# Kernel optimization log

Measured on AMD Instinct MI355X. Metric: run time of the kernel, lower is better.

The kernel has to match this reference:

```python
import jax, jax.numpy as jnp
import numpy as np

B, N, DIM = 2, 2048, 1024
H, DH = 16, 64
INNER = H * DH
LN_EPS = 1e-5
ATTN_EPS = 1e-8
SCALE = DH ** -0.5


def setup_inputs() -> dict:
    key = jax.random.key(0)
    k1, k2, k3 = jax.random.split(key, 3)
    x = jax.random.normal(k1, (B, N, DIM), dtype=jnp.float32)
    ln_gamma = jnp.ones((DIM,), dtype=jnp.float32)
    ln_beta = jnp.zeros((DIM,), dtype=jnp.float32)
    w_qkv = jax.random.normal(k2, (DIM, 3 * INNER), dtype=jnp.float32) * 0.02
    w_out = jax.random.normal(k3, (INNER, DIM), dtype=jnp.float32) * 0.02
    b_out = jnp.zeros((DIM,), dtype=jnp.float32)
    return {"x": x, "ln_gamma": ln_gamma, "ln_beta": ln_beta,
            "w_qkv": w_qkv, "w_out": w_out, "b_out": b_out}


def reference(x, ln_gamma, ln_beta, w_qkv, w_out, b_out):
    # LayerNorm over last dim (biased variance, eps=1e-5)
    mu = jnp.mean(x, axis=-1, keepdims=True)
    var = jnp.var(x, axis=-1, keepdims=True)
    xn = (x - mu) * jax.lax.rsqrt(var + LN_EPS) * ln_gamma + ln_beta
    # QKV projection (no bias), split heads: b n (h d) -> b h n d
    qkv = xn @ w_qkv                                    # [B, N, 3*INNER]
    q, k, v = jnp.split(qkv, 3, axis=-1)
    split_heads = lambda t: t.reshape(B, N, H, DH).transpose(0, 2, 1, 3)
    q, k, v = split_heads(q), split_heads(k), split_heads(v)
    # 'softmax' attn_type: exp(scale * q k^T), normalized by row-sum + eps
    scores = jnp.einsum('bhnd,bhmd->bhnm', q, k) * SCALE   # [B, H, N, N]
    numer = jnp.exp(scores)
    denom = jnp.sum(numer, axis=-1, keepdims=True) + ATTN_EPS
    attn = numer / denom
    out = jnp.einsum('bhnm,bhmd->bhnd', attn, v)           # [B, H, N, DH]
    out = out.transpose(0, 2, 1, 3).reshape(B, N, INNER)   # b h n d -> b n (h d)
    return out @ w_out + b_out
```

## Files before the change

### kernel.cpp

```cpp
#include <hip/hip_runtime.h>
#include <hip/hip_bf16.h>

#define NB    2
#define SEQ   2048
#define DIM_  1024
#define NH    16
#define DHD   64
#define INNER 1024
#define ROWS  4096

typedef _Float16 half_t;
typedef __attribute__((ext_vector_type(4))) _Float16 half4;
typedef __attribute__((ext_vector_type(8))) _Float16 half8;
typedef __attribute__((ext_vector_type(4))) float f32x4;
typedef __attribute__((ext_vector_type(16))) float f32x16;
typedef __attribute__((ext_vector_type(2))) int int2v;
typedef __attribute__((ext_vector_type(4))) int int4v;

__device__ __forceinline__ void async16(const void* g, void* l) {
    __builtin_amdgcn_global_load_lds(
        (const __attribute__((address_space(1))) unsigned int*)g,
        (__attribute__((address_space(3))) unsigned int*)l, 16, 0, 0);
}

__device__ __forceinline__ float ldf(const void* p, size_t i, int isb) {
    if (isb) {
        unsigned int v = ((unsigned int)((const unsigned short*)p)[i]) << 16;
        return __uint_as_float(v);
    }
    return ((const float*)p)[i];
}

__global__ void detect_dtype(const unsigned short* x, int* flag) {
    int tid = threadIdx.x;
    int cnt = 0;
    for (int i = tid; i < 2048; i += 64) {
        float f = __uint_as_float(((unsigned int)x[2 * i]) << 16);
        float a = fabsf(f);
        if (a >= 0.0009765625f && a <= 16.0f) cnt++;
    }
    for (int off = 32; off > 0; off >>= 1) cnt += __shfl_down(cnt, off);
    if (tid == 0) flag[0] = (cnt > 1024) ? 1 : 0;
}

__global__ __launch_bounds__(256) void ln_kernel(const void* __restrict__ x,
                                                 const void* __restrict__ gamma,
                                                 const void* __restrict__ beta,
                                                 half_t* __restrict__ xn,
                                                 const int* __restrict__ flag) {
    int row = blockIdx.x;
    int isb = flag[0];
    int tid = threadIdx.x;
    float vals[4];
    float s = 0.f, ss = 0.f;
    if (!isb) {
        float4 xv = *(const float4*)((const float*)x + (size_t)row * DIM_ + tid * 4);
        vals[0] = xv.x; vals[1] = xv.y; vals[2] = xv.z; vals[3] = xv.w;
    } else {
        #pragma unroll
        for (int j = 0; j < 4; j++) vals[j] = ldf(x, (size_t)row * DIM_ + tid * 4 + j, isb);
    }
    #pragma unroll
    for (int j = 0; j < 4; j++) { s += vals[j]; ss += vals[j] * vals[j]; }
    __shared__ float red[2][4];
    for (int off = 32; off > 0; off >>= 1) {
        s += __shfl_down(s, off);
        ss += __shfl_down(ss, off);
    }
    int wid = tid >> 6;
    if ((tid & 63) == 0) { red[0][wid] = s; red[1][wid] = ss; }
    __syncthreads();
    if (tid == 0) {
        float S = 0.f, SS = 0.f;
        for (int w = 0; w < 4; w++) { S += red[0][w]; SS += red[1][w]; }
        float mu = S / 1024.f;
        float var = SS / 1024.f - mu * mu;
        red[0][0] = mu;
        red[1][0] = rsqrtf(var + 1e-5f);
    }
    __syncthreads();
    float mu = red[0][0], r = red[1][0];
    half4 o;
    #pragma unroll
    for (int j = 0; j < 4; j++) {
        int c = tid * 4 + j;
        float g = ldf(gamma, c, isb);
        float b = ldf(beta, c, isb);
        o[j] = (half_t)((vals[j] - mu) * r * g + b);
    }
    *(half4*)(xn + (size_t)row * DIM_ + tid * 4) = o;
}

__global__ __launch_bounds__(256) void wtrans(const void* __restrict__ W,
                                              half_t* __restrict__ WT,
                                              int K_, int N_,
                                              const int* __restrict__ flag) {
    __shared__ half_t T[64][72];
    int isb = flag[0];
    int k0 = blockIdx.y * 64, n0 = blockIdx.x * 64;
    int t = threadIdx.x;
    if (!isb) {
        #pragma unroll
        for (int p = 0; p < 4; p++) {
            int idx = p * 256 + t;
            int r = idx >> 4, c4 = (idx & 15) * 4;
            float4 xv = *(const float4*)((const float*)W + (size_t)(k0 + r) * N_ + n0 + c4);
            T[r][c4] = (half_t)xv.x; T[r][c4 + 1] = (half_t)xv.y;
            T[r][c4 + 2] = (half_t)xv.z; T[r][c4 + 3] = (half_t)xv.w;
        }
    } else {
        int c = t & 63, rw = t >> 6;
        #pragma unroll
        for (int p = 0; p < 16; p++) {
            int r = p * 4 + rw;
            T[r][c] = (half_t)ldf(W, (size_t)(k0 + r) * N_ + n0 + c, isb);
        }
    }
    __syncthreads();
    int c = t & 63, rw = t >> 6;
    #pragma unroll
    for (int p = 0; p < 16; p++) {
        int r = p * 4 + rw;
        WT[(size_t)(n0 + r) * K_ + k0 + c] = T[c][r];
    }
}

__global__ __launch_bounds__(256) void qkv_gemm(const half_t* __restrict__ A,
                                                const half_t* __restrict__ BT,
                                                half_t* __restrict__ q,
                                                half_t* __restrict__ kp,
                                                half_t* __restrict__ vp) {
    __shared__ half_t As[128 * 64];
    __shared__ half_t Bs[192 * 64];
    int t = threadIdx.x;
    int w = t >> 6, l = t & 63;
    int lm = l & 15, q4 = l >> 4;
    int bid = blockIdx.y * 16 + blockIdx.x;
    int xcd = bid & 7, jj = bid >> 3;
    int r0 = (xcd * 4 + jj / 16) * 128, c0 = (jj % 16) * 192;
    int wr = (w >> 1) * 64, wc = (w & 1) * 96;
    int srow = l >> 3, sg = l & 7;
    f32x4 acc[4][6] = {};
    for (int k0 = 0; k0 < 1024; k0 += 64) {
        __syncthreads();
        int g = sg ^ (srow & 7);
        #pragma unroll
        for (int p = 0; p < 4; p++) {
            int row = p * 32 + w * 8 + srow;
            async16(A + (size_t)(r0 + row) * 1024 + k0 + g * 8, &As[(p * 32 + w * 8) * 64]);
        }
        #pragma unroll
        for (int p = 0; p < 6; p++) {
            int row = p * 32 + w * 8 + srow;
            async16(BT + (size_t)(c0 + row) * 1024 + k0 + g * 8, &Bs[(p * 32 + w * 8) * 64]);
        }
        __syncthreads();
        #pragma unroll
        for (int s = 0; s < 2; s++) {
            int gp = ((s * 4 + q4) ^ (lm & 7)) * 8;
            half8 av[4], bv[6];
            #pragma unroll
            for (int i = 0; i < 4; i++)
                av[i] = *(const half8*)&As[(wr + i * 16 + lm) * 64 + gp];
            #pragma unroll
            for (int j = 0; j < 6; j++)
                bv[j] = *(const half8*)&Bs[(wc + j * 16 + lm) * 64 + gp];
            #pragma unroll
            for (int i = 0; i < 4; i++)
                #pragma unroll
                for (int j = 0; j < 6; j++)
                    acc[i][j] = __builtin_amdgcn_mfma_f32_16x16x32_f16(bv[j], av[i], acc[i][j], 0, 0, 0);
        }
    }
    #pragma unroll
    for (int i = 0; i < 4; i++) {
        int row = r0 + wr + i * 16 + lm;
        int bb = row >> 11, nn = row & 2047;
        #pragma unroll
        for (int j = 0; j < 6; j++) {
            int f0 = c0 + wc + j * 16 + q4 * 4;
            int which = f0 >> 10, within = f0 & 1023;
            int h = within >> 6, d0 = within & 63;
            int bh = bb * NH + h;
            if (which == 0) {
                half4 val;
                #pragma unroll
                for (int r = 0; r < 4; r++) val[r] = (half_t)acc[i][j][r];
                *(half4*)&q[((size_t)bh * SEQ + nn) * DHD + d0] = val;
            } else if (which == 1) {
                int kt = nn >> 7, kb = (nn >> 5) & 3, qi = nn & 31;
                int ks = d0 >> 4, hf = (d0 >> 3) & 1, e = d0 & 7;
                half4 val;
                #pragma unroll
                for (int r = 0; r < 4; r++) val[r] = (half_t)acc[i][j][r];
                size_t off = ((size_t)bh * 16 + kt) * 8192 +
                             (size_t)(((kb * 4 + ks) * 2 + hf) * 32 + qi) * 8 + e;
                *(half4*)&kp[off] = val;
            } else {
                int kt = nn >> 7, k_in = nn & 127;
                int kb = k_in >> 5, c2 = (k_in >> 4) & 1, rem = k_in & 15;
                int hfv = (rem >> 2) & 1, ev = (rem & 3) | ((rem >> 3) << 2);
                size_t bkt = ((size_t)bh * 16 + kt) * 8192;
                #pragma unroll
                for (int r = 0; r < 4; r++) {
                    int d = d0 + r;
                    int mt2 = d >> 5, qi = d & 31;
                    size_t off = bkt +
                        (size_t)((((kb * 2 + c2) * 2 + mt2) * 64 + hfv * 32 + qi) * 8 + ev);
                    vp[off] = (half_t)acc[i][j][r];
                }
            }
        }
    }
}

__global__ __launch_bounds__(256) void out_gemm(const half_t* __restrict__ A,
                                                const half_t* __restrict__ BT,
                                                const void* __restrict__ bias,
                                                void* __restrict__ outp,
                                                const int* __restrict__ flag) {
    __shared__ half_t As[64 * 64];
    __shared__ half_t Bs[128 * 64];
    int isb = flag[0];
    int t = threadIdx.x;
    int w = t >> 6, l = t & 63;
    int lm = l & 15, q4 = l >> 4;
    int bid = blockIdx.y * 8 + blockIdx.x;
    int xcd = bid & 7, jj = bid >> 3;
    int r0 = (xcd * 8 + jj / 8) * 64, c0 = (jj % 8) * 128;
    int wr = (w >> 1) * 32, wc = (w & 1) * 64;
    int srow = l >> 3, sg = l & 7;
    f32x4 acc[2][4] = {};
    for (int k0 = 0; k0 < 1024; k0 += 64) {
        __syncthreads();
        #pragma unroll
        for (int p = 0; p < 2; p++) {
            int row = p * 32 + w * 8 + srow;
            int g = sg ^ (srow & 7);
            async16(A + (size_t)(r0 + row) * 1024 + k0 + g * 8, &As[(p * 32 + w * 8) * 64]);
        }
        #pragma unroll
        for (int p = 0; p < 4; p++) {
            int row = p * 32 + w * 8 + srow;
            int g = sg ^ (srow & 7);
            async16(BT + (size_t)(c0 + row) * 1024 + k0 + g * 8, &Bs[(p * 32 + w * 8) * 64]);
        }
        __syncthreads();
        #pragma unroll
        for (int s = 0; s < 2; s++) {
            int gp = ((s * 4 + q4) ^ (lm & 7)) * 8;
            half8 av[2], bv[4];
            #pragma unroll
            for (int i = 0; i < 2; i++)
                av[i] = *(const half8*)&As[(wr + i * 16 + lm) * 64 + gp];
            #pragma unroll
            for (int j = 0; j < 4; j++)
                bv[j] = *(const half8*)&Bs[(wc + j * 16 + lm) * 64 + gp];
            #pragma unroll
            for (int i = 0; i < 2; i++)
                #pragma unroll
                for (int j = 0; j < 4; j++)
                    acc[i][j] = __builtin_amdgcn_mfma_f32_16x16x32_f16(bv[j], av[i], acc[i][j], 0, 0, 0);
        }
    }
    #pragma unroll
    for (int i = 0; i < 2; i++) {
        int row = r0 + wr + i * 16 + lm;
        #pragma unroll
        for (int j = 0; j < 4; j++) {
            int col0 = c0 + wc + j * 16 + q4 * 4;
            if (!isb) {
                float4 val;
                float* vpp = (float*)&val;
                #pragma unroll
                for (int r = 0; r < 4; r++)
                    vpp[r] = acc[i][j][r] + ((const float*)bias)[col0 + r];
                *(float4*)&((float*)outp)[(size_t)row * DIM_ + col0] = val;
            } else {
                #pragma unroll
                for (int r = 0; r < 4; r++) {
                    float val = acc[i][j][r] + ldf(bias, col0 + r, isb);
                    ((__hip_bfloat16*)outp)[(size_t)row * DIM_ + col0 + r] = __float2bfloat16(val);
                }
            }
        }
    }
}

__global__ __launch_bounds__(512) void attn_mfma(const half_t* __restrict__ q,
                                                 const half_t* __restrict__ kp,
                                                 const half_t* __restrict__ vp,
                                                 half_t* __restrict__ ao) {
    __shared__ __align__(16) char smem[66560];
    int t = threadIdx.x;
    int w = t >> 6, l = t & 63;
    int qi = l & 31, hf = l >> 5;
    int wq = w & 3, wk = w >> 2;
    int bid = blockIdx.x;
    int xcd = bid & 7, jj = bid >> 3;
    int bh = xcd * 4 + (jj >> 3), qt = jj & 7;
    int b = bh >> 4, hd = bh & 15;
    int qrow0 = qt * 256 + wq * 64;

    const char* kpb = (const char*)kp + (size_t)bh * 16 * 16384;
    const char* vpb = (const char*)vp + (size_t)bh * 16 * 16384;

    half8 qf[2][4];
    #pragma unroll
    for (int sq = 0; sq < 2; sq++)
        #pragma unroll
        for (int ks = 0; ks < 4; ks++) {
            qf[sq][ks] = *(const half8*)(q +
                ((size_t)bh * SEQ + qrow0 + sq * 32 + qi) * DHD + ks * 16 + hf * 8);
            qf[sq][ks] *= (_Float16)0.125f;
        }

    f32x16 oacc[2][2] = {};
    float lacc[2] = {0.f, 0.f};

    #pragma unroll
    for (int r = 0; r < 2; r++) {
        async16(kpb + r * 8192 + w * 1024 + l * 16, smem + r * 8192 + w * 1024);
        async16(vpb + r * 8192 + w * 1024 + l * 16, smem + 16384 + r * 8192 + w * 1024);
    }

    for (int kt = 0; kt < 16; kt++) {
        int cur = kt & 1;
        __syncthreads();
        if (kt < 15) {
            const char* kg = kpb + (size_t)(kt + 1) * 16384;
            const char* vg = vpb + (size_t)(kt + 1) * 16384;
            char* dst = smem + (cur ^ 1) * 32768;
            #pragma unroll
            for (int r = 0; r < 2; r++) {
                async16(kg + r * 8192 + w * 1024 + l * 16, dst + r * 8192 + w * 1024);
                async16(vg + r * 8192 + w * 1024 + l * 16, dst + 16384 + r * 8192 + w * 1024);
            }
        }
        const half_t* Kt = (const half_t*)(smem + cur * 32768);
        const half_t* Vt = (const half_t*)(smem + cur * 32768 + 16384);
        half8 kreg[2][4];
        #pragma unroll
        for (int mt = 0; mt < 2; mt++)
            #pragma unroll
            for (int ks = 0; ks < 4; ks++)
                kreg[mt][ks] = *(const half8*)(Kt + ((wk * 2 + mt) * 4 + ks) * 512 + l * 8);
        half8 vreg[2][2][2];
        #pragma unroll
        for (int mt = 0; mt < 2; mt++)
            #pragma unroll
            for (int c = 0; c < 2; c++)
                #pragma unroll
                for (int mt2 = 0; mt2 < 2; mt2++)
                    vreg[mt][c][mt2] = *(const half8*)(Vt +
                        (((wk * 2 + mt) * 2 + c) * 2 + mt2) * 512 + l * 8);
        #pragma unroll
        for (int mt = 0; mt < 2; mt++) {
            #pragma unroll
            for (int sq = 0; sq < 2; sq++) {
                f32x16 sacc = {};
                #pragma unroll
                for (int ks = 0; ks < 4; ks++)
                    sacc = __builtin_amdgcn_mfma_f32_32x32x16_f16(kreg[mt][ks], qf[sq][ks], sacc, 0, 0, 0);
                half4 quads[4];
                #pragma unroll
                for (int g = 0; g < 4; g++) {
                    #pragma unroll
                    for (int s2 = 0; s2 < 4; s2++) {
                        float e = __expf(sacc[g * 4 + s2]);
                        lacc[sq] += e;
                        quads[g][s2] = (half_t)e;
                    }
                }
                #pragma unroll
                for (int c = 0; c < 2; c++) {
                    int2v s0 = __builtin_bit_cast(int2v, quads[2 * c]);
                    int2v s1 = __builtin_bit_cast(int2v, quads[2 * c + 1]);
                    int4v bi;
                    bi.x = s0.x; bi.y = s0.y; bi.z = s1.x; bi.w = s1.y;
                    half8 bfrag = __builtin_bit_cast(half8, bi);
                    #pragma unroll
                    for (int mt2 = 0; mt2 < 2; mt2++)
                        oacc[sq][mt2] = __builtin_amdgcn_mfma_f32_32x32x16_f16(vreg[mt][c][mt2], bfrag, oacc[sq][mt2], 0, 0, 0);
                }
            }
        }
    }
    lacc[0] += __shfl_xor(lacc[0], 32);
    lacc[1] += __shfl_xor(lacc[1], 32);

    __syncthreads();

    float* Osh = (float*)smem;
    float* Lsh = (float*)(smem + 65536);
    if (wk == 1) {
        #pragma unroll
        for (int sq = 0; sq < 2; sq++) {
            #pragma unroll
            for (int mt2 = 0; mt2 < 2; mt2++)
                #pragma unroll
                for (int reg = 0; reg < 16; reg++) {
                    int d = mt2 * 32 + (reg & 3) + 8 * (reg >> 2) + 4 * hf;
                    Osh[(wq * 2 + sq) * 2048 + d * 32 + qi] = oacc[sq][mt2][reg];
                }
            if (hf == 0) Lsh[(wq * 2 + sq) * 32 + qi] = lacc[sq];
        }
    }
    __syncthreads();
    if (wk == 0) {
        #pragma unroll
        for (int sq = 0; sq < 2; sq++) {
            float ltot = lacc[sq] + Lsh[(wq * 2 + sq) * 32 + qi];
            float inv = 1.0f / (ltot + 1e-8f);
            #pragma unroll
            for (int mt2 = 0; mt2 < 2; mt2++)
                #pragma unroll
                for (int r2 = 0; r2 < 4; r2++) {
                    int d0 = mt2 * 32 + 8 * r2 + 4 * hf;
                    half4 ov;
                    #pragma unroll
                    for (int r = 0; r < 4; r++) {
                        float vsum = oacc[sq][mt2][r2 * 4 + r] +
                                     Osh[(wq * 2 + sq) * 2048 + (d0 + r) * 32 + qi];
                        ov[r] = (_Float16)(vsum * inv);
                    }
                    *(half4*)(ao + (size_t)(b * SEQ + qrow0 + sq * 32 + qi) * INNER + hd * 64 + d0) = ov;
                }
        }
    }
}

extern "C" void kernel_launch(void* const* d_in, const int* in_sizes, int n_in,
                              void* d_out, int out_size, void* d_ws, size_t ws_size,
                              hipStream_t stream) {
    const void* x     = d_in[0];
    const void* gamma = d_in[1];
    const void* beta  = d_in[2];
    const void* wqkv  = d_in[3];
    const void* wout  = d_in[4];
    const void* bout  = d_in[5];

    char* ws = (char*)d_ws;
    int*    flag   = (int*)ws;
    half_t* xn16   = (half_t*)(ws + 256);
    half_t* wqkvT  = xn16  + (size_t)4096 * 1024;
    half_t* woutT  = wqkvT + (size_t)3072 * 1024;
    half_t* q16    = woutT + (size_t)1024 * 1024;
    half_t* kp16   = q16   + (size_t)4096 * 1024;
    half_t* vp16   = kp16  + (size_t)4096 * 1024;
    half_t* ao16   = vp16  + (size_t)4096 * 1024;

    detect_dtype<<<1, 64, 0, stream>>>((const unsigned short*)x, flag);
    ln_kernel<<<ROWS, 256, 0, stream>>>(x, gamma, beta, xn16, flag);
    wtrans<<<dim3(48, 16), 256, 0, stream>>>(wqkv, wqkvT, 1024, 3072, flag);
    wtrans<<<dim3(16, 16), 256, 0, stream>>>(wout, woutT, 1024, 1024, flag);
    qkv_gemm<<<dim3(16, 32), 256, 0, stream>>>(xn16, wqkvT, q16, kp16, vp16);
    attn_mfma<<<dim3(256), 512, 0, stream>>>(q16, kp16, vp16, ao16);
    out_gemm<<<dim3(8, 64), 256, 0, stream>>>(ao16, woutT, bout, d_out, flag);
}
```

Before: 190.0 us.

## Split attention into smaller 256-thread blocks with four-way key split per query tile

```diff
diff --git a/kernel.cpp b/kernel.cpp
--- a/kernel.cpp
+++ b/kernel.cpp
@@ -287,20 +287,20 @@
     }
 }
 
-__global__ __launch_bounds__(512) void attn_mfma(const half_t* __restrict__ q,
-                                                 const half_t* __restrict__ kp,
-                                                 const half_t* __restrict__ vp,
-                                                 half_t* __restrict__ ao) {
-    __shared__ __align__(16) char smem[66560];
+__global__ __launch_bounds__(256, 4) void attn_mfma(const half_t* __restrict__ q,
+                                                    const half_t* __restrict__ kp,
+                                                    const half_t* __restrict__ vp,
+                                                    half_t* __restrict__ ao) {
+    __shared__ __align__(16) char smem[33280];
     int t = threadIdx.x;
     int w = t >> 6, l = t & 63;
     int qi = l & 31, hf = l >> 5;
-    int wq = w & 3, wk = w >> 2;
+    int wk = w;
     int bid = blockIdx.x;
     int xcd = bid & 7, jj = bid >> 3;
-    int bh = xcd * 4 + (jj >> 3), qt = jj & 7;
+    int bh = xcd * 4 + (jj >> 5), qt = jj & 31;
     int b = bh >> 4, hd = bh & 15;
-    int qrow0 = qt * 256 + wq * 64;
+    int qrow0 = qt * 64;
 
     const char* kpb = (const char*)kp + (size_t)bh * 16 * 16384;
     const char* vpb = (const char*)vp + (size_t)bh * 16 * 16384;
@@ -318,71 +318,55 @@
     f32x16 oacc[2][2] = {};
     float lacc[2] = {0.f, 0.f};
 
-    #pragma unroll
-    for (int r = 0; r < 2; r++) {
-        async16(kpb + r * 8192 + w * 1024 + l * 16, smem + r * 8192 + w * 1024);
-        async16(vpb + r * 8192 + w * 1024 + l * 16, smem + 16384 + r * 8192 + w * 1024);
-    }
-
     for (int kt = 0; kt < 16; kt++) {
-        int cur = kt & 1;
-        __syncthreads();
-        if (kt < 15) {
-            const char* kg = kpb + (size_t)(kt + 1) * 16384;
-            const char* vg = vpb + (size_t)(kt + 1) * 16384;
-            char* dst = smem + (cur ^ 1) * 32768;
-            #pragma unroll
-            for (int r = 0; r < 2; r++) {
-                async16(kg + r * 8192 + w * 1024 + l * 16, dst + r * 8192 + w * 1024);
-                async16(vg + r * 8192 + w * 1024 + l * 16, dst + 16384 + r * 8192 + w * 1024);
+        __syncthreads();
+        const char* kg = kpb + (size_t)kt * 16384;
+        const char* vg = vpb + (size_t)kt * 16384;
+        #pragma unroll
+        for (int r = 0; r < 4; r++) {
+            async16(kg + r * 4096 + w * 1024 + l * 16, smem + r * 4096 + w * 1024);
+            async16(vg + r * 4096 + w * 1024 + l * 16, smem + 16384 + r * 4096 + w * 1024);
+        }
+        __syncthreads();
+        const half_t* Kt = (const half_t*)smem;
+        const half_t* Vt = (const half_t*)(smem + 16384);
+        half8 kreg[4];
+        #pragma unroll
+        for (int ks = 0; ks < 4; ks++)
+            kreg[ks] = *(const half8*)(Kt + (wk * 4 + ks) * 512 + l * 8);
+        half8 vreg[2][2];
+        #pragma unroll
+        for (int c = 0; c < 2; c++)
+            #pragma unroll
+            for (int mt2 = 0; mt2 < 2; mt2++)
+                vreg[c][mt2] = *(const half8*)(Vt +
+                    ((wk * 2 + c) * 2 + mt2) * 512 + l * 8);
+        #pragma unroll
+        for (int sq = 0; sq < 2; sq++) {
+            f32x16 sacc = {};
+            #pragma unroll
+            for (int ks = 0; ks < 4; ks++)
+                sacc = __builtin_amdgcn_mfma_f32_32x32x16_f16(kreg[ks], qf[sq][ks], sacc, 0, 0, 0);
+            half4 quads[4];
+            #pragma unroll
+            for (int g = 0; g < 4; g++) {
+                #pragma unroll
+                for (int s2 = 0; s2 < 4; s2++) {
+                    float e = __expf(sacc[g * 4 + s2]);
+                    lacc[sq] += e;
+                    quads[g][s2] = (half_t)e;
+                }
             }
-        }
-        const half_t* Kt = (const half_t*)(smem + cur * 32768);
-        const half_t* Vt = (const half_t*)(smem + cur * 32768 + 16384);
-        half8 kreg[2][4];
-        #pragma unroll
-        for (int mt = 0; mt < 2; mt++)
-            #pragma unroll
-            for (int ks = 0; ks < 4; ks++)
-                kreg[mt][ks] = *(const half8*)(Kt + ((wk * 2 + mt) * 4 + ks) * 512 + l * 8);
-        half8 vreg[2][2][2];
-        #pragma unroll
-        for (int mt = 0; mt < 2; mt++)
-            #pragma unroll
-            for (int c = 0; c < 2; c++)
+            #pragma unroll
+            for (int c = 0; c < 2; c++) {
+                int2v s0 = __builtin_bit_cast(int2v, quads[2 * c]);
+                int2v s1 = __builtin_bit_cast(int2v, quads[2 * c + 1]);
+                int4v bi;
+                bi.x = s0.x; bi.y = s0.y; bi.z = s1.x; bi.w = s1.y;
+                half8 bfrag = __builtin_bit_cast(half8, bi);
                 #pragma unroll
                 for (int mt2 = 0; mt2 < 2; mt2++)
-                    vreg[mt][c][mt2] = *(const half8*)(Vt +
-                        (((wk * 2 + mt) * 2 + c) * 2 + mt2) * 512 + l * 8);
-        #pragma unroll
-        for (int mt = 0; mt < 2; mt++) {
-            #pragma unroll
-            for (int sq = 0; sq < 2; sq++) {
-                f32x16 sacc = {};
-                #pragma unroll
-                for (int ks = 0; ks < 4; ks++)
-                    sacc = __builtin_amdgcn_mfma_f32_32x32x16_f16(kreg[mt][ks], qf[sq][ks], sacc, 0, 0, 0);
-                half4 quads[4];
-                #pragma unroll
-                for (int g = 0; g < 4; g++) {
-                    #pragma unroll
-                    for (int s2 = 0; s2 < 4; s2++) {
-                        float e = __expf(sacc[g * 4 + s2]);
-                        lacc[sq] += e;
-                        quads[g][s2] = (half_t)e;
-                    }
-                }
-                #pragma unroll
-                for (int c = 0; c < 2; c++) {
-                    int2v s0 = __builtin_bit_cast(int2v, quads[2 * c]);
-                    int2v s1 = __builtin_bit_cast(int2v, quads[2 * c + 1]);
-                    int4v bi;
-                    bi.x = s0.x; bi.y = s0.y; bi.z = s1.x; bi.w = s1.y;
-                    half8 bfrag = __builtin_bit_cast(half8, bi);
-                    #pragma unroll
-                    for (int mt2 = 0; mt2 < 2; mt2++)
-                        oacc[sq][mt2] = __builtin_amdgcn_mfma_f32_32x32x16_f16(vreg[mt][c][mt2], bfrag, oacc[sq][mt2], 0, 0, 0);
-                }
+                    oacc[sq][mt2] = __builtin_amdgcn_mfma_f32_32x32x16_f16(vreg[c][mt2], bfrag, oacc[sq][mt2], 0, 0, 0);
             }
         }
     }
@@ -392,8 +376,9 @@
     __syncthreads();
 
     float* Osh = (float*)smem;
-    float* Lsh = (float*)(smem + 65536);
-    if (wk == 1) {
+    float* Lsh = (float*)(smem + 32768);
+    if (wk >= 2) {
+        int buf = wk - 2;
         #pragma unroll
         for (int sq = 0; sq < 2; sq++) {
             #pragma unroll
@@ -401,16 +386,45 @@
                 #pragma unroll
                 for (int reg = 0; reg < 16; reg++) {
                     int d = mt2 * 32 + (reg & 3) + 8 * (reg >> 2) + 4 * hf;
-                    Osh[(wq * 2 + sq) * 2048 + d * 32 + qi] = oacc[sq][mt2][reg];
-                }
-            if (hf == 0) Lsh[(wq * 2 + sq) * 32 + qi] = lacc[sq];
+                    Osh[(buf * 2 + sq) * 2048 + d * 32 + qi] = oacc[sq][mt2][reg];
+                }
+            if (hf == 0) Lsh[(buf * 2 + sq) * 32 + qi] = lacc[sq];
+        }
+    }
+    __syncthreads();
+    if (wk < 2) {
+        int buf = wk;
+        #pragma unroll
+        for (int sq = 0; sq < 2; sq++) {
+            #pragma unroll
+            for (int mt2 = 0; mt2 < 2; mt2++)
+                #pragma unroll
+                for (int reg = 0; reg < 16; reg++) {
+                    int d = mt2 * 32 + (reg & 3) + 8 * (reg >> 2) + 4 * hf;
+                    oacc[sq][mt2][reg] += Osh[(buf * 2 + sq) * 2048 + d * 32 + qi];
+                }
+            lacc[sq] += Lsh[(buf * 2 + sq) * 32 + qi];
+        }
+    }
+    __syncthreads();
+    if (wk == 1) {
+        #pragma unroll
+        for (int sq = 0; sq < 2; sq++) {
+            #pragma unroll
+            for (int mt2 = 0; mt2 < 2; mt2++)
+                #pragma unroll
+                for (int reg = 0; reg < 16; reg++) {
+                    int d = mt2 * 32 + (reg & 3) + 8 * (reg >> 2) + 4 * hf;
+                    Osh[sq * 2048 + d * 32 + qi] = oacc[sq][mt2][reg];
+                }
+            if (hf == 0) Lsh[sq * 32 + qi] = lacc[sq];
         }
     }
     __syncthreads();
     if (wk == 0) {
         #pragma unroll
         for (int sq = 0; sq < 2; sq++) {
-            float ltot = lacc[sq] + Lsh[(wq * 2 + sq) * 32 + qi];
+            float ltot = lacc[sq] + Lsh[sq * 32 + qi];
             float inv = 1.0f / (ltot + 1e-8f);
             #pragma unroll
             for (int mt2 = 0; mt2 < 2; mt2++)
@@ -421,7 +435,7 @@
                     #pragma unroll
                     for (int r = 0; r < 4; r++) {
                         float vsum = oacc[sq][mt2][r2 * 4 + r] +
-                                     Osh[(wq * 2 + sq) * 2048 + (d0 + r) * 32 + qi];
+                                     Osh[sq * 2048 + (d0 + r) * 32 + qi];
                         ov[r] = (_Float16)(vsum * inv);
                     }
                     *(half4*)(ao + (size_t)(b * SEQ + qrow0 + sq * 32 + qi) * INNER + hd * 64 + d0) = ov;
@@ -455,6 +469,6 @@
     wtrans<<<dim3(48, 16), 256, 0, stream>>>(wqkv, wqkvT, 1024, 3072, flag);
     wtrans<<<dim3(16, 16), 256, 0, stream>>>(wout, woutT, 1024, 1024, flag);
     qkv_gemm<<<dim3(16, 32), 256, 0, stream>>>(xn16, wqkvT, q16, kp16, vp16);
-    attn_mfma<<<dim3(256), 512, 0, stream>>>(q16, kp16, vp16, ao16);
+    attn_mfma<<<dim3(1024), 256, 0, stream>>>(q16, kp16, vp16, ao16);
     out_gemm<<<dim3(8, 64), 256, 0, stream>>>(ao16, woutT, bout, d_out, flag);
 }
```

Measured after the change: 250.9 us. 1.32x slower.

## Split attention key tiles across four wave groups and double grid size

Applied to the files above, without the earlier changes.

```diff
diff --git a/kernel.cpp b/kernel.cpp
--- a/kernel.cpp
+++ b/kernel.cpp
@@ -287,20 +287,20 @@
     }
 }
 
-__global__ __launch_bounds__(512) void attn_mfma(const half_t* __restrict__ q,
-                                                 const half_t* __restrict__ kp,
-                                                 const half_t* __restrict__ vp,
-                                                 half_t* __restrict__ ao) {
+__global__ __launch_bounds__(512, 4) void attn_mfma(const half_t* __restrict__ q,
+                                                    const half_t* __restrict__ kp,
+                                                    const half_t* __restrict__ vp,
+                                                    half_t* __restrict__ ao) {
     __shared__ __align__(16) char smem[66560];
     int t = threadIdx.x;
     int w = t >> 6, l = t & 63;
     int qi = l & 31, hf = l >> 5;
-    int wq = w & 3, wk = w >> 2;
+    int wq = w & 1, wk = w >> 1;
     int bid = blockIdx.x;
     int xcd = bid & 7, jj = bid >> 3;
-    int bh = xcd * 4 + (jj >> 3), qt = jj & 7;
+    int bh = xcd * 4 + (jj >> 4), qt = jj & 15;
     int b = bh >> 4, hd = bh & 15;
-    int qrow0 = qt * 256 + wq * 64;
+    int qrow0 = qt * 128 + wq * 64;
 
     const char* kpb = (const char*)kp + (size_t)bh * 16 * 16384;
     const char* vpb = (const char*)vp + (size_t)bh * 16 * 16384;
@@ -339,50 +339,43 @@
         }
         const half_t* Kt = (const half_t*)(smem + cur * 32768);
         const half_t* Vt = (const half_t*)(smem + cur * 32768 + 16384);
-        half8 kreg[2][4];
-        #pragma unroll
-        for (int mt = 0; mt < 2; mt++)
+        half8 kreg[4];
+        #pragma unroll
+        for (int ks = 0; ks < 4; ks++)
+            kreg[ks] = *(const half8*)(Kt + (wk * 4 + ks) * 512 + l * 8);
+        half8 vreg[2][2];
+        #pragma unroll
+        for (int c = 0; c < 2; c++)
+            #pragma unroll
+            for (int mt2 = 0; mt2 < 2; mt2++)
+                vreg[c][mt2] = *(const half8*)(Vt +
+                    ((wk * 2 + c) * 2 + mt2) * 512 + l * 8);
+        #pragma unroll
+        for (int sq = 0; sq < 2; sq++) {
+            f32x16 sacc = {};
             #pragma unroll
             for (int ks = 0; ks < 4; ks++)
-                kreg[mt][ks] = *(const half8*)(Kt + ((wk * 2 + mt) * 4 + ks) * 512 + l * 8);
-        half8 vreg[2][2][2];
-        #pragma unroll
-        for (int mt = 0; mt < 2; mt++)
-            #pragma unroll
-            for (int c = 0; c < 2; c++)
+                sacc = __builtin_amdgcn_mfma_f32_32x32x16_f16(kreg[ks], qf[sq][ks], sacc, 0, 0, 0);
+            half4 quads[4];
+            #pragma unroll
+            for (int g = 0; g < 4; g++) {
+                #pragma unroll
+                for (int s2 = 0; s2 < 4; s2++) {
+                    float e = __expf(sacc[g * 4 + s2]);
+                    lacc[sq] += e;
+                    quads[g][s2] = (half_t)e;
+                }
+            }
+            #pragma unroll
+            for (int c = 0; c < 2; c++) {
+                int2v s0 = __builtin_bit_cast(int2v, quads[2 * c]);
+                int2v s1 = __builtin_bit_cast(int2v, quads[2 * c + 1]);
+                int4v bi;
+                bi.x = s0.x; bi.y = s0.y; bi.z = s1.x; bi.w = s1.y;
+                half8 bfrag = __builtin_bit_cast(half8, bi);
                 #pragma unroll
                 for (int mt2 = 0; mt2 < 2; mt2++)
-                    vreg[mt][c][mt2] = *(const half8*)(Vt +
-                        (((wk * 2 + mt) * 2 + c) * 2 + mt2) * 512 + l * 8);
-        #pragma unroll
-        for (int mt = 0; mt < 2; mt++) {
-            #pragma unroll
-            for (int sq = 0; sq < 2; sq++) {
-                f32x16 sacc = {};
-                #pragma unroll
-                for (int ks = 0; ks < 4; ks++)
-                    sacc = __builtin_amdgcn_mfma_f32_32x32x16_f16(kreg[mt][ks], qf[sq][ks], sacc, 0, 0, 0);
-                half4 quads[4];
-                #pragma unroll
-                for (int g = 0; g < 4; g++) {
-                    #pragma unroll
-                    for (int s2 = 0; s2 < 4; s2++) {
-                        float e = __expf(sacc[g * 4 + s2]);
-                        lacc[sq] += e;
-                        quads[g][s2] = (half_t)e;
-                    }
-                }
-                #pragma unroll
-                for (int c = 0; c < 2; c++) {
-                    int2v s0 = __builtin_bit_cast(int2v, quads[2 * c]);
-                    int2v s1 = __builtin_bit_cast(int2v, quads[2 * c + 1]);
-                    int4v bi;
-                    bi.x = s0.x; bi.y = s0.y; bi.z = s1.x; bi.w = s1.y;
-                    half8 bfrag = __builtin_bit_cast(half8, bi);
-                    #pragma unroll
-                    for (int mt2 = 0; mt2 < 2; mt2++)
-                        oacc[sq][mt2] = __builtin_amdgcn_mfma_f32_32x32x16_f16(vreg[mt][c][mt2], bfrag, oacc[sq][mt2], 0, 0, 0);
-                }
+                    oacc[sq][mt2] = __builtin_amdgcn_mfma_f32_32x32x16_f16(vreg[c][mt2], bfrag, oacc[sq][mt2], 0, 0, 0);
             }
         }
     }
@@ -393,6 +386,36 @@
 
     float* Osh = (float*)smem;
     float* Lsh = (float*)(smem + 65536);
+    if (wk >= 2) {
+        int buf = wk - 2;
+        #pragma unroll
+        for (int sq = 0; sq < 2; sq++) {
+            #pragma unroll
+            for (int mt2 = 0; mt2 < 2; mt2++)
+                #pragma unroll
+                for (int reg = 0; reg < 16; reg++) {
+                    int d = mt2 * 32 + (reg & 3) + 8 * (reg >> 2) + 4 * hf;
+                    Osh[((buf * 2 + wq) * 2 + sq) * 2048 + d * 32 + qi] = oacc[sq][mt2][reg];
+                }
+            if (hf == 0) Lsh[((buf * 2 + wq) * 2 + sq) * 32 + qi] = lacc[sq];
+        }
+    }
+    __syncthreads();
+    if (wk < 2) {
+        int buf = wk;
+        #pragma unroll
+        for (int sq = 0; sq < 2; sq++) {
+            #pragma unroll
+            for (int mt2 = 0; mt2 < 2; mt2++)
+                #pragma unroll
+                for (int reg = 0; reg < 16; reg++) {
+                    int d = mt2 * 32 + (reg & 3) + 8 * (reg >> 2) + 4 * hf;
+                    oacc[sq][mt2][reg] += Osh[((buf * 2 + wq) * 2 + sq) * 2048 + d * 32 + qi];
+                }
+            lacc[sq] += Lsh[((buf * 2 + wq) * 2 + sq) * 32 + qi];
+        }
+    }
+    __syncthreads();
     if (wk == 1) {
         #pragma unroll
         for (int sq = 0; sq < 2; sq++) {
@@ -455,6 +478,6 @@
     wtrans<<<dim3(48, 16), 256, 0, stream>>>(wqkv, wqkvT, 1024, 3072, flag);
     wtrans<<<dim3(16, 16), 256, 0, stream>>>(wout, woutT, 1024, 1024, flag);
     qkv_gemm<<<dim3(16, 32), 256, 0, stream>>>(xn16, wqkvT, q16, kp16, vp16);
-    attn_mfma<<<dim3(256), 512, 0, stream>>>(q16, kp16, vp16, ao16);
+    attn_mfma<<<dim3(512), 512, 0, stream>>>(q16, kp16, vp16, ao16);
     out_gemm<<<dim3(8, 64), 256, 0, stream>>>(ao16, woutT, bout, d_out, flag);
 }
```

Measured after the change: 254.9 us. +34.2%, slower.
